# Optimization experiments

Hardware: AMD Instinct MI355X
Metric: run time of the kernel (lower is better)

## Reference

```python
import jax, jax.numpy as jnp
import numpy as np

N = 50000        # nodes
E = 800000       # edges per meta-path (avg degree 16)
M = 3            # meta-paths
IN = 256         # in_size
HID = 16         # hidden_size (per-head out dim of GATConv)
HEADS = 8
OUT = 8          # out_size (classes)
SA_HID = 128     # StructureAttention hidden_size default
NEG_SLOPE = 0.2  # DGL GATConv leaky_relu default


def setup_inputs() -> dict:
    key = jax.random.key(0)
    ks = jax.random.split(key, 11)
    h = jax.random.normal(ks[0], (N, IN), jnp.float32)
    edges = jax.random.randint(ks[1], (M, 2, E), 0, N, jnp.int32)  # [M, (src,dst), E]
    s = 0.05
    fc_w = jax.random.normal(ks[2], (M, IN, HEADS * HID), jnp.float32) * s
    attn_l = jax.random.normal(ks[3], (M, HEADS, HID), jnp.float32) * s
    attn_r = jax.random.normal(ks[4], (M, HEADS, HID), jnp.float32) * s
    sa_w1 = jax.random.normal(ks[5], (HEADS * HID, SA_HID), jnp.float32) * s
    sa_b1 = jnp.zeros((SA_HID,), jnp.float32)
    sa_w2 = jax.random.normal(ks[6], (SA_HID, 1), jnp.float32) * s
    pred_w = jax.random.normal(ks[7], (HEADS * HID, OUT), jnp.float32) * s
    pred_b = jnp.zeros((OUT,), jnp.float32)
    return {"h": h, "edges": edges, "fc_w": fc_w, "attn_l": attn_l,
            "attn_r": attn_r, "sa_w1": sa_w1, "sa_b1": sa_b1, "sa_w2": sa_w2,
            "pred_w": pred_w, "pred_b": pred_b}


def _gat(h, src, dst, w, al, ar):
    # DGL GATConv, eval mode (dropout=0), activation=elu
    feat = (h @ w).reshape(N, HEADS, HID)                 # [N,H,D]
    el = jnp.einsum('nhd,hd->nh', feat, al)               # [N,H]
    er = jnp.einsum('nhd,hd->nh', feat, ar)               # [N,H]
    e = el[src] + er[dst]                                 # [E,H]
    e = jnp.where(e > 0, e, NEG_SLOPE * e)                # leaky_relu
    # edge softmax over incoming edges of each dst node
    emax = jax.ops.segment_max(e, dst, num_segments=N)    # [N,H]
    ex = jnp.exp(e - emax[dst])                           # [E,H]
    denom = jax.ops.segment_sum(ex, dst, num_segments=N)  # [N,H]
    alpha = ex / denom[dst]                               # [E,H]
    msg = feat[src] * alpha[:, :, None]                   # [E,H,D]
    out = jax.ops.segment_sum(msg, dst, num_segments=N)   # [N,H,D]
    return jax.nn.elu(out).reshape(N, HEADS * HID)        # flatten(1)


def reference(h, edges, fc_w, attn_l, attn_r, sa_w1, sa_b1, sa_w2, pred_w, pred_b):
    # per-meta-path GAT (loop over fixed small set of meta-paths)
    zs = [_gat(h, edges[i, 0], edges[i, 1], fc_w[i], attn_l[i], attn_r[i])
          for i in range(M)]
    z = jnp.stack(zs, axis=1)                             # [N, M, H*D]
    # StructureAttention exactly as in source: softmax over dim 0 (nodes)
    w = jnp.tanh(z @ sa_w1 + sa_b1) @ sa_w2               # [N, M, 1]
    beta = jax.nn.softmax(w, axis=0)                      # softmax over nodes
    fused = (beta * z).sum(0)                             # [M, H*D]
    return fused @ pred_w + pred_b                        # [M, OUT]
```

## Files before the change

kernel.cpp:

```cpp
#include <hip/hip_runtime.h>

#define N_NODES 50000
#define N_EDGES 800000
#define N_META 3
#define IN_DIM 256
#define HD 128
#define HEADS 8
#define HID 16
#define OUT_DIM 8
#define NBKT 196
#define BCAP 5120
#define TILE_E 4096
#define GEMM_BX ((N_NODES + 63) / 64)
#define ELER_BX ((N_NODES * HEADS + 255) / 256)
#define BING_NB (3 * NBKT)
#define PSTRIDE 132

using bf16x8 = __attribute__((ext_vector_type(8))) short;
using f32x4  = __attribute__((ext_vector_type(4))) float;

__device__ __forceinline__ float bf2f(unsigned short u) {
  union { unsigned int i; float f; } x; x.i = ((unsigned int)u) << 16; return x.f;
}
__device__ __forceinline__ unsigned short f2bf(float f) {
  union { float f; unsigned int i; } x; x.f = f;
  unsigned int r = x.i + 0x7fffu + ((x.i >> 16) & 1u);
  return (unsigned short)(r >> 16);
}
__device__ __forceinline__ float tanh_fast(float x) {
  float e = __expf(2.f * x);
  return 1.f - 2.f / (e + 1.f);
}

__global__ __launch_bounds__(256)
void prep_kernel(const float* __restrict__ fcw, const float* __restrict__ w1,
                 unsigned short* __restrict__ fcwT, unsigned short* __restrict__ w1T,
                 int* __restrict__ gcur) {
  int i = blockIdx.x * 256 + threadIdx.x;
  const int NFC = N_META * IN_DIM * HD;
  const int NW1 = HD * HD;
  const int NGC = N_META * NBKT;
  if (i < NFC) {
    int p = i / (IN_DIM * HD);
    int rem = i - p * (IN_DIM * HD);
    int k = rem / HD, n = rem - k * HD;
    fcwT[(size_t)p * HD * IN_DIM + n * IN_DIM + k] = f2bf(fcw[i]);
  } else if (i < NFC + NW1) {
    int j = i - NFC;
    int k = j / HD, n = j - k * HD;
    w1T[n * HD + k] = f2bf(w1[j]);
  } else if (i < NFC + NW1 + NGC) {
    gcur[i - NFC - NW1] = 0;
  }
}

__global__ __launch_bounds__(256)
void bin_kernel(const int* __restrict__ edges, int* __restrict__ gcur,
                unsigned int* __restrict__ bktbuf) {
  __shared__ int hist[NBKT];
  __shared__ int gbase[NBKT];
  __shared__ int fill[NBKT];
  int t = threadIdx.x;
  int bx = blockIdx.x;
  int p = bx / NBKT;
  int b = bx - p * NBKT;
  int e0 = b * TILE_E;
  const int* src = edges + (size_t)p * 2 * N_EDGES;
  const int* dst = src + N_EDGES;
  for (int i = t; i < NBKT; i += 256) { hist[i] = 0; fill[i] = 0; }
  __syncthreads();
  for (int i = t; i < TILE_E; i += 256) {
    int e = e0 + i;
    if (e < N_EDGES) atomicAdd(&hist[dst[e] >> 8], 1);
  }
  __syncthreads();
  for (int i = t; i < NBKT; i += 256) {
    int idx = p * NBKT + i;
    gbase[i] = hist[i] ? (idx * BCAP + atomicAdd(&gcur[idx], hist[i])) : 0;
  }
  __syncthreads();
  for (int i = t; i < TILE_E; i += 256) {
    int e = e0 + i;
    if (e < N_EDGES) {
      int d = dst[e];
      int b2 = d >> 8;
      int r = atomicAdd(&fill[b2], 1);
      bktbuf[gbase[b2] + r] = ((unsigned int)(d & 255) << 16) | (unsigned int)src[e];
    }
  }
}

__global__ __launch_bounds__(256)
void gemm_kernel(const float* __restrict__ A,
                 const unsigned short* __restrict__ BT,
                 unsigned short* __restrict__ Cb, int nrows) {
  __shared__ unsigned short As[64 * 40];
  __shared__ unsigned short Bs[384 * 40];
  int t = threadIdx.x;
  int w = t >> 6, l = t & 63, q = l >> 4, s = l & 15;
  int row0 = blockIdx.x * 64;
  f32x4 acc[4][6] = {};
  for (int k0 = 0; k0 < IN_DIM; k0 += 32) {
    {
      int r = t >> 2, c = (t & 3) * 8;
      int gr = row0 + r;
      float4 a0, a1;
      if (gr < nrows) {
        a0 = *(const float4*)(A + (size_t)gr * IN_DIM + k0 + c);
        a1 = *(const float4*)(A + (size_t)gr * IN_DIM + k0 + c + 4);
      } else {
        a0 = make_float4(0.f, 0.f, 0.f, 0.f); a1 = a0;
      }
      ushort4 u0, u1;
      u0.x = f2bf(a0.x); u0.y = f2bf(a0.y); u0.z = f2bf(a0.z); u0.w = f2bf(a0.w);
      u1.x = f2bf(a1.x); u1.y = f2bf(a1.y); u1.z = f2bf(a1.z); u1.w = f2bf(a1.w);
      *(ushort4*)&As[r * 40 + c]     = u0;
      *(ushort4*)&As[r * 40 + c + 4] = u1;
    }
    {
      int n = t >> 1, c = (t & 1) * 16;
      #pragma unroll
      for (int mm = 0; mm < 3; ++mm) {
        const unsigned short* BTm =
            BT + (size_t)mm * HD * IN_DIM + (size_t)n * IN_DIM + k0 + c;
        uint4 b0 = *(const uint4*)(BTm);
        uint4 b1 = *(const uint4*)(BTm + 8);
        unsigned short* Bsm = Bs + (mm * 128 + n) * 40 + c;
        *(uint4*)&Bsm[0] = b0;
        *(uint4*)&Bsm[8] = b1;
      }
    }
    __syncthreads();
    bf16x8 bfv[6];
    #pragma unroll
    for (int nt = 0; nt < 6; ++nt)
      bfv[nt] = *(bf16x8*)&Bs[(w * 96 + nt * 16 + s) * 40 + q * 8];
    #pragma unroll
    for (int mt = 0; mt < 4; ++mt) {
      bf16x8 af = *(bf16x8*)&As[(mt * 16 + s) * 40 + q * 8];
      #pragma unroll
      for (int nt = 0; nt < 6; ++nt)
        acc[mt][nt] = __builtin_amdgcn_mfma_f32_16x16x32_bf16(af, bfv[nt], acc[mt][nt], 0, 0, 0);
    }
    __syncthreads();
  }
  #pragma unroll
  for (int mt = 0; mt < 4; ++mt) {
    #pragma unroll
    for (int nt = 0; nt < 6; ++nt) {
      int gc = w * 96 + nt * 16 + s;
      int mm = gc >> 7, cim = gc & 127;
      unsigned short* Cm = Cb + (size_t)mm * N_NODES * HD;
      #pragma unroll
      for (int r = 0; r < 4; ++r) {
        int gr = row0 + mt * 16 + q * 4 + r;
        if (gr < nrows) Cm[(size_t)gr * HD + cim] = f2bf(acc[mt][nt][r]);
      }
    }
  }
}

__global__ __launch_bounds__(256)
void sort_eler_kernel(const int* __restrict__ gcur,
                      const unsigned int* __restrict__ bktbuf,
                      int* __restrict__ offsB, int* __restrict__ offsE,
                      int* __restrict__ csr,
                      const unsigned short* __restrict__ featb3,
                      const float* __restrict__ al, const float* __restrict__ ar,
                      float* __restrict__ el3, float* __restrict__ er3) {
  __shared__ int lh[256];
  __shared__ int cur[256];
  __shared__ int wsum[4];
  int p = blockIdx.y;
  int t = threadIdx.x;
  if (blockIdx.x < NBKT) {
    int b = blockIdx.x;
    int lane = t & 63, wid = t >> 6;
    int idx = p * NBKT + b;
    int S = idx * BCAP;
    int E = S + gcur[idx];
    int node0 = b * 256;
    int nn = min(256, N_NODES - node0);
    int gi0 = p * N_NODES + node0;
    lh[t] = 0;
    __syncthreads();
    for (int i = S + t; i < E; i += 256) atomicAdd(&lh[bktbuf[i] >> 16], 1);
    __syncthreads();
    int v = lh[t];
    int s = v;
    #pragma unroll
    for (int d = 1; d < 64; d <<= 1) {
      int x = __shfl_up(s, d);
      if (lane >= d) s += x;
    }
    if (lane == 63) wsum[wid] = s;
    __syncthreads();
    int woff = 0;
    #pragma unroll
    for (int k = 0; k < 4; ++k) if (k < wid) woff += wsum[k];
    int excl = S + woff + s - v;
    if (t < nn) {
      offsB[gi0 + t] = excl;
      offsE[gi0 + t] = excl + v;
    }
    cur[t] = excl;
    __syncthreads();
    for (int i = S + t; i < E; i += 256) {
      unsigned int rec = bktbuf[i];
      int pos = atomicAdd(&cur[rec >> 16], 1);
      csr[pos] = (int)(rec & 0xffffu);
    }
  } else {
    int i = (blockIdx.x - NBKT) * 256 + t;
    if (i >= N_NODES * HEADS) return;
    int node = i >> 3, hh = i & 7;
    const unsigned short* f =
        featb3 + (size_t)p * N_NODES * HD + (size_t)node * HD + hh * HID;
    uint4 u0 = *(const uint4*)(f);
    uint4 u1 = *(const uint4*)(f + 8);
    unsigned int uu[8] = {u0.x, u0.y, u0.z, u0.w, u1.x, u1.y, u1.z, u1.w};
    const float* alm = al + p * HD + hh * HID;
    const float* arm = ar + p * HD + hh * HID;
    float sl = 0.f, sr = 0.f;
    #pragma unroll
    for (int q = 0; q < 8; ++q) {
      float v0 = __uint_as_float(uu[q] << 16);
      float v1 = __uint_as_float(uu[q] & 0xffff0000u);
      int d = q * 2;
      sl += v0 * alm[d] + v1 * alm[d + 1];
      sr += v0 * arm[d] + v1 * arm[d + 1];
    }
    el3[(size_t)p * N_NODES * HEADS + i] = sl;
    er3[(size_t)p * N_NODES * HEADS + i] = sr;
  }
}

__global__ __launch_bounds__(256)
void aggregate_kernel(const int* __restrict__ offsB3, const int* __restrict__ offsE3,
                      const int* __restrict__ csr,
                      const uint4* __restrict__ featb3_u4,
                      const float* __restrict__ el3, const float* __restrict__ er3,
                      uint4* __restrict__ zb3_u4, int m) {
  int node = blockIdx.x * 4 + (threadIdx.x >> 6);
  if (node >= N_NODES) return;
  const uint4* featb_u4 = featb3_u4 + (size_t)m * N_NODES * 16;
  const float* el = el3 + (size_t)m * N_NODES * HEADS;
  const float* er = er3 + (size_t)m * N_NODES * HEADS;
  uint4* z_u4 = zb3_u4 + (size_t)m * N_NODES * 16;
  int lane = threadIdx.x & 63;
  int qg = lane >> 4;
  int li = lane & 15;
  int ch = li >> 1;
  int beg = offsB3[m * N_NODES + node], end = offsE3[m * N_NODES + node];
  float erh = er[node * HEADS + ch];
  float ssum = 0.f;
  float a[8] = {};
  for (int i = beg; i < end; i += 16) {
    int nk = end - i;
    int last = end - 1;
    int s0 = csr[min(i + qg,      last)];
    int s1 = csr[min(i + qg + 4,  last)];
    int s2 = csr[min(i + qg + 8,  last)];
    int s3 = csr[min(i + qg + 12, last)];
    uint4 v0 = featb_u4[(size_t)s0 * 16 + li];
    uint4 v1 = featb_u4[(size_t)s1 * 16 + li];
    uint4 v2 = featb_u4[(size_t)s2 * 16 + li];
    uint4 v3 = featb_u4[(size_t)s3 * 16 + li];
    float e0 = el[s0 * HEADS + ch] + erh;
    float e1 = el[s1 * HEADS + ch] + erh;
    float e2 = el[s2 * HEADS + ch] + erh;
    float e3 = el[s3 * HEADS + ch] + erh;
    e0 = e0 > 0.f ? e0 : 0.2f * e0;
    e1 = e1 > 0.f ? e1 : 0.2f * e1;
    e2 = e2 > 0.f ? e2 : 0.2f * e2;
    e3 = e3 > 0.f ? e3 : 0.2f * e3;
    float w0 = (qg      < nk) ? __expf(e0) : 0.f;
    float w1 = (qg + 4  < nk) ? __expf(e1) : 0.f;
    float w2 = (qg + 8  < nk) ? __expf(e2) : 0.f;
    float w3 = (qg + 12 < nk) ? __expf(e3) : 0.f;
    ssum += (w0 + w1) + (w2 + w3);
    a[0] += w0 * __uint_as_float(v0.x << 16);
    a[1] += w0 * __uint_as_float(v0.x & 0xffff0000u);
    a[2] += w0 * __uint_as_float(v0.y << 16);
    a[3] += w0 * __uint_as_float(v0.y & 0xffff0000u);
    a[4] += w0 * __uint_as_float(v0.z << 16);
    a[5] += w0 * __uint_as_float(v0.z & 0xffff0000u);
    a[6] += w0 * __uint_as_float(v0.w << 16);
    a[7] += w0 * __uint_as_float(v0.w & 0xffff0000u);
    a[0] += w1 * __uint_as_float(v1.x << 16);
    a[1] += w1 * __uint_as_float(v1.x & 0xffff0000u);
    a[2] += w1 * __uint_as_float(v1.y << 16);
    a[3] += w1 * __uint_as_float(v1.y & 0xffff0000u);
    a[4] += w1 * __uint_as_float(v1.z << 16);
    a[5] += w1 * __uint_as_float(v1.z & 0xffff0000u);
    a[6] += w1 * __uint_as_float(v1.w << 16);
    a[7] += w1 * __uint_as_float(v1.w & 0xffff0000u);
    a[0] += w2 * __uint_as_float(v2.x << 16);
    a[1] += w2 * __uint_as_float(v2.x & 0xffff0000u);
    a[2] += w2 * __uint_as_float(v2.y << 16);
    a[3] += w2 * __uint_as_float(v2.y & 0xffff0000u);
    a[4] += w2 * __uint_as_float(v2.z << 16);
    a[5] += w2 * __uint_as_float(v2.z & 0xffff0000u);
    a[6] += w2 * __uint_as_float(v2.w << 16);
    a[7] += w2 * __uint_as_float(v2.w & 0xffff0000u);
    a[0] += w3 * __uint_as_float(v3.x << 16);
    a[1] += w3 * __uint_as_float(v3.x & 0xffff0000u);
    a[2] += w3 * __uint_as_float(v3.y << 16);
    a[3] += w3 * __uint_as_float(v3.y & 0xffff0000u);
    a[4] += w3 * __uint_as_float(v3.z << 16);
    a[5] += w3 * __uint_as_float(v3.z & 0xffff0000u);
    a[6] += w3 * __uint_as_float(v3.w << 16);
    a[7] += w3 * __uint_as_float(v3.w & 0xffff0000u);
  }
  #pragma unroll
  for (int j = 0; j < 8; ++j) {
    a[j] += __shfl_xor(a[j], 16);
    a[j] += __shfl_xor(a[j], 32);
  }
  ssum += __shfl_xor(ssum, 16);
  ssum += __shfl_xor(ssum, 32);
  float inv = (end > beg) ? 1.f / ssum : 0.f;
  if (qg == 0) {
    #pragma unroll
    for (int j = 0; j < 8; ++j) {
      float z = a[j] * inv;
      a[j] = z > 0.f ? z : __expf(z) - 1.f;
    }
    uint4 o;
    unsigned int p0, p1, p2, p3;
    asm("v_cvt_pk_bf16_f32 %0, %1, %2" : "=v"(p0) : "v"(a[0]), "v"(a[1]));
    asm("v_cvt_pk_bf16_f32 %0, %1, %2" : "=v"(p1) : "v"(a[2]), "v"(a[3]));
    asm("v_cvt_pk_bf16_f32 %0, %1, %2" : "=v"(p2) : "v"(a[4]), "v"(a[5]));
    asm("v_cvt_pk_bf16_f32 %0, %1, %2" : "=v"(p3) : "v"(a[6]), "v"(a[7]));
    o.x = p0; o.y = p1; o.z = p2; o.w = p3;
    z_u4[(size_t)node * 16 + li] = o;
  }
}

__global__ __launch_bounds__(256)
void w_gemm_mfma(const unsigned short* __restrict__ Zb3,
                 const unsigned short* __restrict__ BT,
                 const float* __restrict__ B1, const float* __restrict__ W2,
                 float* __restrict__ partial, int nrows) {
  __shared__ unsigned short Bs[128 * 128];
  __shared__ float ew[64];
  __shared__ float part[4][64][2];
  int tid = threadIdx.x;
  int m = blockIdx.y;
  const unsigned short* Zb = Zb3 + (size_t)m * N_NODES * HD;
  int w = tid >> 6, l = tid & 63, q = l >> 4, s = l & 15;
  int row0 = blockIdx.x * 64;
  {
    int n = tid >> 1;
    int jb = (tid & 1) * 8;
    #pragma unroll
    for (int jj = 0; jj < 8; ++jj) {
      int j = jb + jj;
      *(uint4*)&Bs[n * 128 + ((j ^ (n & 15)) << 3)] =
          *(const uint4*)(BT + n * HD + j * 8);
    }
  }
  float b1v[8], w2v[8];
  #pragma unroll
  for (int f = 0; f < 8; ++f) { b1v[f] = B1[f * 16 + s]; w2v[f] = W2[f * 16 + s]; }
  int gra = min(row0 + w * 16 + s, nrows - 1);
  const unsigned short* arow = Zb + (size_t)gra * HD;
  bf16x8 af[4];
  #pragma unroll
  for (int kc = 0; kc < 4; ++kc)
    af[kc] = *(const bf16x8*)(arow + kc * 32 + q * 8);
  __syncthreads();
  f32x4 acc[8] = {};
  #pragma unroll
  for (int kc = 0; kc < 4; ++kc) {
    #pragma unroll
    for (int f = 0; f < 8; ++f) {
      bf16x8 bf = *(bf16x8*)&Bs[(f * 16 + s) * 128 + ((((kc << 2) | q) ^ s) << 3)];
      acc[f] = __builtin_amdgcn_mfma_f32_16x16x32_bf16(af[kc], bf, acc[f], 0, 0, 0);
    }
  }
  #pragma unroll
  for (int r = 0; r < 4; ++r) {
    float p = 0.f;
    #pragma unroll
    for (int f = 0; f < 8; ++f) p += tanh_fast(acc[f][r] + b1v[f]) * w2v[f];
    p += __shfl_xor(p, 1); p += __shfl_xor(p, 2);
    p += __shfl_xor(p, 4); p += __shfl_xor(p, 8);
    if (s == 0) {
      int rr = w * 16 + q * 4 + r;
      ew[rr] = (row0 + rr < nrows) ? __expf(p) : 0.f;
    }
  }
  __syncthreads();
  const unsigned int* Zu = (const unsigned int*)Zb;
  int rmax = min(64, nrows - row0);
  float a0 = 0.f, a1 = 0.f;
  for (int r = w; r < rmax; r += 4) {
    float e = ew[r];
    unsigned int v = Zu[(size_t)(row0 + r) * 64 + l];
    a0 += e * __uint_as_float(v << 16);
    a1 += e * __uint_as_float(v & 0xffff0000u);
  }
  part[w][l][0] = a0;
  part[w][l][1] = a1;
  __syncthreads();
  if (w == 0) {
    float s0 = part[0][l][0] + part[1][l][0] + part[2][l][0] + part[3][l][0];
    float s1 = part[0][l][1] + part[1][l][1] + part[2][l][1] + part[3][l][1];
    float* prow = partial + ((size_t)m * GEMM_BX + blockIdx.x) * PSTRIDE;
    prow[2 * l]     = s0;
    prow[2 * l + 1] = s1;
    float ldv = ew[l];
    ldv += __shfl_xor(ldv, 1);  ldv += __shfl_xor(ldv, 2);
    ldv += __shfl_xor(ldv, 4);  ldv += __shfl_xor(ldv, 8);
    ldv += __shfl_xor(ldv, 16); ldv += __shfl_xor(ldv, 32);
    if (l == 0) prow[128] = ldv;
  }
}

__global__ __launch_bounds__(256)
void reduce_final_kernel(const float* __restrict__ partial,
                         const float* __restrict__ PW, const float* __restrict__ PB,
                         float* __restrict__ out) {
  __shared__ float num[129];
  int m = blockIdx.x;
  int t = threadIdx.x;
  if (t < 129) {
    const float* base = partial + (size_t)m * GEMM_BX * PSTRIDE + t;
    float a0 = 0.f, a1 = 0.f, a2 = 0.f, a3 = 0.f;
    int b = 0;
    for (; b + 4 <= GEMM_BX; b += 4) {
      a0 += base[(size_t)(b + 0) * PSTRIDE];
      a1 += base[(size_t)(b + 1) * PSTRIDE];
      a2 += base[(size_t)(b + 2) * PSTRIDE];
      a3 += base[(size_t)(b + 3) * PSTRIDE];
    }
    for (; b < GEMM_BX; ++b) a0 += base[(size_t)b * PSTRIDE];
    num[t] = (a0 + a1) + (a2 + a3);
  }
  __syncthreads();
  if (t < OUT_DIM) {
    float inv = 1.f / num[128];
    float s = 0.f;
    for (int k = 0; k < HD; ++k) s += num[k] * PW[k * OUT_DIM + t];
    out[m * OUT_DIM + t] = s * inv + PB[t];
  }
}

extern "C" void kernel_launch(void* const* d_in, const int* in_sizes, int n_in,
                              void* d_out, int out_size, void* d_ws, size_t ws_size,
                              hipStream_t stream) {
  (void)in_sizes; (void)n_in; (void)out_size; (void)ws_size;
  const float* h     = (const float*)d_in[0];
  const int*   edges = (const int*)d_in[1];
  const float* fcw   = (const float*)d_in[2];
  const float* al    = (const float*)d_in[3];
  const float* ar    = (const float*)d_in[4];
  const float* w1    = (const float*)d_in[5];
  const float* b1    = (const float*)d_in[6];
  const float* w2    = (const float*)d_in[7];
  const float* pw    = (const float*)d_in[8];
  const float* pb    = (const float*)d_in[9];
  float* out = (float*)d_out;

  char* ws = (char*)d_ws;
  size_t off = 0;
  auto alloc = [&](size_t bytes) -> void* {
    void* p = ws + off;
    off = (off + bytes + 255) & ~(size_t)255;
    return p;
  };
  unsigned short* featb3 = (unsigned short*)alloc((size_t)N_META * N_NODES * HD * 2);
  unsigned short* zb3    = (unsigned short*)alloc((size_t)N_META * N_NODES * HD * 2);
  unsigned short* fcwT   = (unsigned short*)alloc((size_t)N_META * HD * IN_DIM * 2);
  unsigned short* w1T    = (unsigned short*)alloc((size_t)HD * HD * 2);
  float* el3 = (float*)alloc((size_t)N_META * N_NODES * HEADS * 4);
  float* er3 = (float*)alloc((size_t)N_META * N_NODES * HEADS * 4);
  int* gcur  = (int*)alloc((size_t)N_META * NBKT * 4);
  int* offsB = (int*)alloc((size_t)N_META * N_NODES * 4);
  int* offsE = (int*)alloc((size_t)N_META * N_NODES * 4);
  unsigned int* bktbuf = (unsigned int*)alloc((size_t)N_META * NBKT * BCAP * 4);
  int* csr   = (int*)alloc((size_t)N_META * NBKT * BCAP * 4);
  float* partial = (float*)alloc((size_t)N_META * GEMM_BX * PSTRIDE * 4);

  const int PREP_N = N_META * IN_DIM * HD + HD * HD + N_META * NBKT;
  prep_kernel<<<(PREP_N + 255) / 256, 256, 0, stream>>>(
      fcw, w1, fcwT, w1T, gcur);

  bin_kernel<<<BING_NB, 256, 0, stream>>>(edges, gcur, bktbuf);
  gemm_kernel<<<GEMM_BX, 256, 0, stream>>>(h, fcwT, featb3, N_NODES);

  dim3 bgrid_(NBKT + ELER_BX, N_META);
  sort_eler_kernel<<<bgrid_, 256, 0, stream>>>(
      gcur, bktbuf, offsB, offsE, csr, featb3, al, ar, el3, er3);

  for (int mm = 0; mm < N_META; ++mm) {
    aggregate_kernel<<<(N_NODES + 3) / 4, 256, 0, stream>>>(
        offsB, offsE, csr, (const uint4*)featb3, el3, er3, (uint4*)zb3, mm);
  }

  dim3 wgrid((N_NODES + 63) / 64, N_META);
  w_gemm_mfma<<<wgrid, 256, 0, stream>>>(zb3, w1T, b1, w2, partial, N_NODES);

  reduce_final_kernel<<<N_META, 256, 0, stream>>>(partial, pw, pb, out);
}
```

Before: 346.4 us.

## Drop LDS staging in projection GEMM, load fragments directly from global

The feature-projection GEMM no longer stages A and B tiles through shared memory with barriers. Each wave now loads its bf16 weight fragments and fp32 input fragments straight from global memory into registers, and the row tile is halved to 32 so twice as many blocks run. The partial-buffer indexing is split off into its own constant so the later reduction kernels keep their 64-row grid. In exchange, weight fragments are reloaded from global or cache by every block and wave, and input rows are re-read by all four waves, with no sharing between them.

```diff
diff --git a/kernel.cpp b/kernel.cpp
--- a/kernel.cpp
+++ b/kernel.cpp
@@ -11,7 +11,8 @@
 #define NBKT 196
 #define BCAP 5120
 #define TILE_E 4096
-#define GEMM_BX ((N_NODES + 63) / 64)
+#define GEMM_BX ((N_NODES + 31) / 32)
+#define WG_BX   ((N_NODES + 63) / 64)
 #define ELER_BX ((N_NODES * HEADS + 255) / 256)
 #define BING_NB (3 * NBKT)
 #define PSTRIDE 132
@@ -94,58 +95,52 @@
 void gemm_kernel(const float* __restrict__ A,
                  const unsigned short* __restrict__ BT,
                  unsigned short* __restrict__ Cb, int nrows) {
-  __shared__ unsigned short As[64 * 40];
-  __shared__ unsigned short Bs[384 * 40];
   int t = threadIdx.x;
   int w = t >> 6, l = t & 63, q = l >> 4, s = l & 15;
-  int row0 = blockIdx.x * 64;
-  f32x4 acc[4][6] = {};
-  for (int k0 = 0; k0 < IN_DIM; k0 += 32) {
+  int row0 = blockIdx.x * 32;
+  const unsigned short* Bw = BT + (size_t)(w * 96) * IN_DIM;
+  int gr0 = min(row0 + s,      nrows - 1);
+  int gr1 = min(row0 + 16 + s, nrows - 1);
+  const float* ap0 = A + (size_t)gr0 * IN_DIM + q * 8;
+  const float* ap1 = A + (size_t)gr1 * IN_DIM + q * 8;
+  f32x4 acc[2][6] = {};
+  #pragma unroll 2
+  for (int kc = 0; kc < 8; ++kc) {
+    int k0 = kc * 32;
+    bf16x8 af[2];
     {
-      int r = t >> 2, c = (t & 3) * 8;
-      int gr = row0 + r;
-      float4 a0, a1;
-      if (gr < nrows) {
-        a0 = *(const float4*)(A + (size_t)gr * IN_DIM + k0 + c);
-        a1 = *(const float4*)(A + (size_t)gr * IN_DIM + k0 + c + 4);
-      } else {
-        a0 = make_float4(0.f, 0.f, 0.f, 0.f); a1 = a0;
-      }
+      float4 a0 = *(const float4*)(ap0 + k0);
+      float4 a1 = *(const float4*)(ap0 + k0 + 4);
+      union { bf16x8 v; ushort4 u[2]; } cv;
       ushort4 u0, u1;
       u0.x = f2bf(a0.x); u0.y = f2bf(a0.y); u0.z = f2bf(a0.z); u0.w = f2bf(a0.w);
       u1.x = f2bf(a1.x); u1.y = f2bf(a1.y); u1.z = f2bf(a1.z); u1.w = f2bf(a1.w);
-      *(ushort4*)&As[r * 40 + c]     = u0;
-      *(ushort4*)&As[r * 40 + c + 4] = u1;
+      cv.u[0] = u0; cv.u[1] = u1;
+      af[0] = cv.v;
     }
     {
-      int n = t >> 1, c = (t & 1) * 16;
-      #pragma unroll
-      for (int mm = 0; mm < 3; ++mm) {
-        const unsigned short* BTm =
-            BT + (size_t)mm * HD * IN_DIM + (size_t)n * IN_DIM + k0 + c;
-        uint4 b0 = *(const uint4*)(BTm);
-        uint4 b1 = *(const uint4*)(BTm + 8);
-        unsigned short* Bsm = Bs + (mm * 128 + n) * 40 + c;
-        *(uint4*)&Bsm[0] = b0;
-        *(uint4*)&Bsm[8] = b1;
-      }
-    }
-    __syncthreads();
+      float4 a0 = *(const float4*)(ap1 + k0);
+      float4 a1 = *(const float4*)(ap1 + k0 + 4);
+      union { bf16x8 v; ushort4 u[2]; } cv;
+      ushort4 u0, u1;
+      u0.x = f2bf(a0.x); u0.y = f2bf(a0.y); u0.z = f2bf(a0.z); u0.w = f2bf(a0.w);
+      u1.x = f2bf(a1.x); u1.y = f2bf(a1.y); u1.z = f2bf(a1.z); u1.w = f2bf(a1.w);
+      cv.u[0] = u0; cv.u[1] = u1;
+      af[1] = cv.v;
+    }
     bf16x8 bfv[6];
     #pragma unroll
     for (int nt = 0; nt < 6; ++nt)
-      bfv[nt] = *(bf16x8*)&Bs[(w * 96 + nt * 16 + s) * 40 + q * 8];
-    #pragma unroll
-    for (int mt = 0; mt < 4; ++mt) {
-      bf16x8 af = *(bf16x8*)&As[(mt * 16 + s) * 40 + q * 8];
+      bfv[nt] = *(const bf16x8*)(Bw + (size_t)(nt * 16 + s) * IN_DIM + k0 + q * 8);
+    #pragma unroll
+    for (int mt = 0; mt < 2; ++mt) {
       #pragma unroll
       for (int nt = 0; nt < 6; ++nt)
-        acc[mt][nt] = __builtin_amdgcn_mfma_f32_16x16x32_bf16(af, bfv[nt], acc[mt][nt], 0, 0, 0);
-    }
-    __syncthreads();
+        acc[mt][nt] = __builtin_amdgcn_mfma_f32_16x16x32_bf16(af[mt], bfv[nt], acc[mt][nt], 0, 0, 0);
+    }
   }
   #pragma unroll
-  for (int mt = 0; mt < 4; ++mt) {
+  for (int mt = 0; mt < 2; ++mt) {
     #pragma unroll
     for (int nt = 0; nt < 6; ++nt) {
       int gc = w * 96 + nt * 16 + s;
@@ -407,7 +402,7 @@
   if (w == 0) {
     float s0 = part[0][l][0] + part[1][l][0] + part[2][l][0] + part[3][l][0];
     float s1 = part[0][l][1] + part[1][l][1] + part[2][l][1] + part[3][l][1];
-    float* prow = partial + ((size_t)m * GEMM_BX + blockIdx.x) * PSTRIDE;
+    float* prow = partial + ((size_t)m * WG_BX + blockIdx.x) * PSTRIDE;
     prow[2 * l]     = s0;
     prow[2 * l + 1] = s1;
     float ldv = ew[l];
@@ -426,16 +421,16 @@
   int m = blockIdx.x;
   int t = threadIdx.x;
   if (t < 129) {
-    const float* base = partial + (size_t)m * GEMM_BX * PSTRIDE + t;
+    const float* base = partial + (size_t)m * WG_BX * PSTRIDE + t;
     float a0 = 0.f, a1 = 0.f, a2 = 0.f, a3 = 0.f;
     int b = 0;
-    for (; b + 4 <= GEMM_BX; b += 4) {
+    for (; b + 4 <= WG_BX; b += 4) {
       a0 += base[(size_t)(b + 0) * PSTRIDE];
       a1 += base[(size_t)(b + 1) * PSTRIDE];
       a2 += base[(size_t)(b + 2) * PSTRIDE];
       a3 += base[(size_t)(b + 3) * PSTRIDE];
     }
-    for (; b < GEMM_BX; ++b) a0 += base[(size_t)b * PSTRIDE];
+    for (; b < WG_BX; ++b) a0 += base[(size_t)b * PSTRIDE];
     num[t] = (a0 + a1) + (a2 + a3);
   }
   __syncthreads();
@@ -481,7 +476,7 @@
   int* offsE = (int*)alloc((size_t)N_META * N_NODES * 4);
   unsigned int* bktbuf = (unsigned int*)alloc((size_t)N_META * NBKT * BCAP * 4);
   int* csr   = (int*)alloc((size_t)N_META * NBKT * BCAP * 4);
-  float* partial = (float*)alloc((size_t)N_META * GEMM_BX * PSTRIDE * 4);
+  float* partial = (float*)alloc((size_t)N_META * WG_BX * PSTRIDE * 4);
 
   const int PREP_N = N_META * IN_DIM * HD + HD * HD + N_META * NBKT;
   prep_kernel<<<(PREP_N + 255) / 256, 256, 0, stream>>>(
```

Measured after the change: 377.3 us. 8.9% more time.
